# Optimization experiments

Hardware: AMD Instinct MI355X
Metric: run time of the kernel (lower is better)

The kernel has to match this reference:

```python
import jax, jax.numpy as jnp
import numpy as np

K = 9      # num_classes
A = 6      # anchors per location (A1 == A2 == 6)
C = 256    # fpn_out_channels


def conv3x3(x, w, b):
    # x: [N,C,H,W], w: [O,I,3,3], b: [O]
    y = jax.lax.conv_general_dilated(
        x, w, window_strides=(1, 1), padding='SAME',
        dimension_numbers=('NCHW', 'OIHW', 'NCHW'))
    return y + b[None, :, None, None]


def setup_inputs() -> dict:
    key = jax.random.key(0)
    ks = jax.random.split(key, 16)
    shapes = [(16, C, 64, 64), (16, C, 32, 32), (16, C, 16, 16),
              (16, C, 8, 8), (16, C, 4, 4), (16, C, 2, 2)]
    inp = {f'feat{i}': jax.random.normal(ks[i], s, dtype=jnp.float32)
           for i, s in enumerate(shapes)}
    # head 1 (used for pyramid levels 0,1) and head 2 (levels >=2)
    inp['w_reg1'] = jax.random.normal(ks[6], (4 * A, C, 3, 3), jnp.float32) * 0.05
    inp['b_reg1'] = jnp.zeros((4 * A,), jnp.float32)
    inp['w_cls1'] = jax.random.normal(ks[7], (K * A, C, 3, 3), jnp.float32) * 0.05
    inp['b_cls1'] = jnp.zeros((K * A,), jnp.float32)
    inp['w_reg2'] = jax.random.normal(ks[8], (4 * A, C, 3, 3), jnp.float32) * 0.05
    inp['b_reg2'] = jnp.zeros((4 * A,), jnp.float32)
    inp['w_cls2'] = jax.random.normal(ks[9], (K * A, C, 3, 3), jnp.float32) * 0.05
    inp['b_cls2'] = jnp.zeros((K * A,), jnp.float32)
    return inp


def reference(feat0, feat1, feat2, feat3, feat4, feat5,
              w_reg1, b_reg1, w_cls1, b_cls1,
              w_reg2, b_reg2, w_cls2, b_cls2):
    feats = [feat0, feat1, feat2, feat3, feat4, feat5]
    locations, confidences = [], []
    for i, x in enumerate(feats):
        if i < 2:
            wr, br, wc, bc = w_reg1, b_reg1, w_cls1, b_cls1
        else:
            wr, br, wc, bc = w_reg2, b_reg2, w_cls2, b_cls2
        n = x.shape[0]
        bbox_delta = conv3x3(x, wr, br).reshape(n, 4, -1)   # [N,4,A*H*W]
        bbox_conf = conv3x3(x, wc, bc).reshape(n, K, -1)    # [N,K,A*H*W]
        locations.append(bbox_delta)
        confidences.append(bbox_conf)
    bbox_delta = jnp.concatenate(locations, axis=2)
    confs = jnp.concatenate(confidences, axis=2)
    return bbox_delta, confs
```

## Files before the change

### kernel.cpp

```cpp
#include <hip/hip_runtime.h>
#include <hip/hip_bf16.h>


typedef float  f32x4  __attribute__((ext_vector_type(4)));
typedef short  bf16x8 __attribute__((ext_vector_type(8)));
typedef int    i32x4  __attribute__((ext_vector_type(4)));

#define TOTAL_ANCH 32760
#define BBOX_TOTAL 2096640
#define PW_BYTES   1474560
#define NB_MAIN    683

__device__ __forceinline__ unsigned short f2bf(float f) {
    unsigned u = __float_as_uint(f);
    return (unsigned short)((u + 0x7FFFu + ((u >> 16) & 1u)) >> 16);
}

__device__ __forceinline__ unsigned pack2(float a, float b) {
    return (unsigned)f2bf(a) | ((unsigned)f2bf(b) << 16);
}

__device__ __forceinline__ void gload16(const void* g, void* l) {
    __builtin_amdgcn_global_load_lds(
        (const __attribute__((address_space(1))) void*)g,
        (__attribute__((address_space(3))) void*)l, 16, 0, 0);
}

__global__ void retina_prepack(
    const float* __restrict__ wr1, const float* __restrict__ br1,
    const float* __restrict__ wc1, const float* __restrict__ bc1,
    const float* __restrict__ wr2, const float* __restrict__ br2,
    const float* __restrict__ wc2, const float* __restrict__ bc2,
    unsigned short* __restrict__ PW, float* __restrict__ PB)
{
    int g = blockIdx.x * 256 + threadIdx.x;
    if (g < 737280) {
        int e = g & 7;
        int b = (g >> 3) & 7;
        int q = g >> 6;
        int o = q % 80;
        int rest = q / 80;
        int kw = rest % 3; rest /= 3;
        int kh = rest % 3; rest /= 3;
        int chunk = rest & 3;
        int head  = rest >> 2;
        float v = 0.f;
        if (o < 78) {
            int c = (chunk << 6) + ((b ^ (o & 7)) << 3) + e;
            const float* wsrc; int oo;
            if (o < 24) { wsrc = head ? wr2 : wr1; oo = o; }
            else        { wsrc = head ? wc2 : wc1; oo = o - 24; }
            v = wsrc[((oo * 256 + c) * 3 + kh) * 3 + kw];
        }
        PW[g] = f2bf(v);
    }
    if (g < 160) {
        int head = g / 80, o = g % 80;
        float bv = 0.f;
        if (o < 24)      bv = (head ? br2 : br1)[o];
        else if (o < 78) bv = (head ? bc2 : bc1)[o - 24];
        PB[g] = bv;
    }
}

__global__ __launch_bounds__(256, 2) void retina_main(
    const float* __restrict__ f0, const float* __restrict__ f1,
    const float* __restrict__ f2, const float* __restrict__ f3,
    const float* __restrict__ f4, const float* __restrict__ f5,
    const unsigned short* __restrict__ PW, const float* __restrict__ PB,
    float* __restrict__ out)
{
    __shared__ __align__(16) char lds[32768 + 2 * 10240];

    const int tid = threadIdx.x;
    const int bid = blockIdx.x;

    int lvl, tile;
    if      (bid < 512) { lvl = 0; tile = bid;       }
    else if (bid < 640) { lvl = 1; tile = bid - 512; }
    else if (bid < 672) { lvl = 2; tile = bid - 640; }
    else if (bid < 680) { lvl = 3; tile = bid - 672; }
    else if (bid < 682) { lvl = 4; tile = bid - 680; }
    else                { lvl = 5; tile = 0;         }

    const int logW  = 6 - lvl;
    const int W     = 1 << logW;
    const int H     = W;
    const int logHW = 2 * logW;
    const int HW    = 1 << logHW;
    const int NHW   = 16 << logHW;

    const int nrowsTab[6] = {4, 6, 10, 18, 34, 34};
    const int offlTab[6]  = {0, 24576, 30720, 32256, 32640, 32736};
    const int S    = nrowsTab[lvl];
    const int offl = offlTab[lvl];
    const float* x = (lvl == 0) ? f0 : (lvl == 1) ? f1 : (lvl == 2) ? f2
                   : (lvl == 3) ? f3 : (lvl == 4) ? f4 : f5;
    const int head = (lvl < 2) ? 0 : 1;

    const int p0 = tile << 7;
    const int r0 = p0 >> logW;

    const int l   = tid & 63;
    const int wv  = tid >> 6;
    const int lg  = l >> 4;
    const int l16 = l & 15;

    int rlocal[2], wpos[2], hrow[2];
    #pragma unroll
    for (int nt = 0; nt < 2; ++nt) {
        int tpos   = wv * 32 + nt * 16 + l16;
        rlocal[nt] = tpos >> logW;
        wpos[nt]   = tpos & (W - 1);
        hrow[nt]   = (r0 + rlocal[nt]) & (H - 1);
    }

    f32x4 acc[5][2];
    {
        f32x4 zf = {0.f, 0.f, 0.f, 0.f};
        #pragma unroll
        for (int m = 0; m < 5; ++m) { acc[m][0] = zf; acc[m][1] = zf; }
    }

    const int axor  = l16 & 7;
    const int aoff0 = l16 * 128 + ((lg       ^ axor) << 4);
    const int aoff1 = l16 * 128 + (((4 + lg) ^ axor) << 4);

    const char* pwbase = (const char*)PW + (size_t)head * 368640;

    auto stageW = [&](int cidx, int buf) {
        const char* src = pwbase + (size_t)cidx * 10240 + wv * 2560 + l * 16;
        char*       dst = lds + 32768 + buf * 10240 + wv * 2560;
        gload16(src,        dst);
        gload16(src + 1024, dst + 1024);
        if (l < 32) gload16(src + 2048, dst + 2048);
    };

    auto stageX = [&](int chunk) {
        const int items = S << (logW + 3);
        for (int e = tid; e < items; e += 256) {
            int w = e & (W - 1);
            int b = (e >> logW) & 7;
            int s = e >> (logW + 3);
            int vr = r0 - 1 + s;
            i32x4 val = {0, 0, 0, 0};
            if ((unsigned)vr < (unsigned)(16 << logW)) {
                int n  = vr >> logW;
                int h  = vr & (H - 1);
                int c0 = (chunk << 6) + (b << 3);
                const float* src = x + (size_t)(((n << 8) + c0) << logHW) + (h << logW) + w;
                float v0 = src[0];          float v1 = src[(size_t)HW];
                float v2 = src[(size_t)2*HW]; float v3 = src[(size_t)3*HW];
                float v4 = src[(size_t)4*HW]; float v5 = src[(size_t)5*HW];
                float v6 = src[(size_t)6*HW]; float v7 = src[(size_t)7*HW];
                val[0] = (int)pack2(v0, v1);
                val[1] = (int)pack2(v2, v3);
                val[2] = (int)pack2(v4, v5);
                val[3] = (int)pack2(v6, v7);
            }
            int rowidx = (s << logW) + w;
            int boff   = rowidx * 128 + ((b ^ (rowidx & 7)) << 4);
            *(i32x4*)(lds + boff) = val;
        }
    };

    stageW(0, 0);
    stageX(0);
    __syncthreads();

    for (int chunk = 0; chunk < 4; ++chunk) {
        if (chunk) { stageX(chunk); __syncthreads(); }
        #pragma unroll
        for (int t9 = 0; t9 < 9; ++t9) {
            const int kh   = t9 / 3;
            const int kw   = t9 % 3;
            const int cidx = chunk * 9 + t9;

            if (cidx + 1 < 36) stageW(cidx + 1, (cidx + 1) & 1);

            bf16x8 bfr[2][2];
            #pragma unroll
            for (int nt = 0; nt < 2; ++nt) {
                int wp  = wpos[nt] + kw - 1;
                bool ok = ((unsigned)(hrow[nt] + kh - 1) < (unsigned)H)
                       && ((unsigned)wp < (unsigned)W);
                int wc = wp < 0 ? 0 : (wp >= W ? W - 1 : wp);
                int rowidx = ((rlocal[nt] + kh) << logW) + wc;
                int rsw = rowidx & 7;
                const char* bp = lds + rowidx * 128;
                bfr[nt][0] = *(const bf16x8*)(bp + ((lg       ^ rsw) << 4));
                bfr[nt][1] = *(const bf16x8*)(bp + (((4 + lg) ^ rsw) << 4));
                if (!ok) {
                    bf16x8 z = {0, 0, 0, 0, 0, 0, 0, 0};
                    bfr[nt][0] = z;
                    bfr[nt][1] = z;
                }
            }

            const char* wb = lds + 32768 + (cidx & 1) * 10240;
            #pragma unroll
            for (int m = 0; m < 5; ++m) {
                bf16x8 a0 = *(const bf16x8*)(wb + m * 2048 + aoff0);
                bf16x8 a1 = *(const bf16x8*)(wb + m * 2048 + aoff1);
                acc[m][0] = __builtin_amdgcn_mfma_f32_16x16x32_bf16(a0, bfr[0][0], acc[m][0], 0, 0, 0);
                acc[m][0] = __builtin_amdgcn_mfma_f32_16x16x32_bf16(a1, bfr[0][1], acc[m][0], 0, 0, 0);
                acc[m][1] = __builtin_amdgcn_mfma_f32_16x16x32_bf16(a0, bfr[1][0], acc[m][1], 0, 0, 0);
                acc[m][1] = __builtin_amdgcn_mfma_f32_16x16x32_bf16(a1, bfr[1][1], acc[m][1], 0, 0, 0);
            }
            __syncthreads();
        }
    }

    const float* bias = PB + head * 80;
    #pragma unroll
    for (int nt = 0; nt < 2; ++nt) {
        int pos = p0 + wv * 32 + nt * 16 + l16;
        if (pos >= NHW) continue;
        int n   = pos >> logHW;
        int rem = pos & (HW - 1);
        int base0 = offl + rem;
        #pragma unroll
        for (int m = 0; m < 5; ++m) {
            #pragma unroll
            for (int r = 0; r < 4; ++r) {
                int o = m * 16 + lg * 4 + r;
                if (o < 78) {
                    float v = acc[m][nt][r] + bias[o];
                    int idx;
                    if (o < 24) {
                        int g = o / 6, a = o - g * 6;
                        idx = (n * 4 + g) * TOTAL_ANCH + base0 + (a << logHW);
                    } else {
                        int cc = o - 24;
                        int k = cc / 6, a = cc - k * 6;
                        idx = BBOX_TOTAL + (n * 9 + k) * TOTAL_ANCH + base0 + (a << logHW);
                    }
                    out[idx] = v;
                }
            }
        }
    }
}

extern "C" void kernel_launch(void* const* d_in, const int* in_sizes, int n_in,
                              void* d_out, int out_size, void* d_ws, size_t ws_size,
                              hipStream_t stream) {
    const float* f0  = (const float*)d_in[0];
    const float* f1  = (const float*)d_in[1];
    const float* f2  = (const float*)d_in[2];
    const float* f3  = (const float*)d_in[3];
    const float* f4  = (const float*)d_in[4];
    const float* f5  = (const float*)d_in[5];
    const float* wr1 = (const float*)d_in[6];
    const float* br1 = (const float*)d_in[7];
    const float* wc1 = (const float*)d_in[8];
    const float* bc1 = (const float*)d_in[9];
    const float* wr2 = (const float*)d_in[10];
    const float* br2 = (const float*)d_in[11];
    const float* wc2 = (const float*)d_in[12];
    const float* bc2 = (const float*)d_in[13];

    unsigned short* PW = (unsigned short*)d_ws;
    float*          PB = (float*)((char*)d_ws + PW_BYTES);

    retina_prepack<<<2880, 256, 0, stream>>>(wr1, br1, wc1, bc1, wr2, br2, wc2, bc2, PW, PB);
    retina_main<<<NB_MAIN, 256, 0, stream>>>(f0, f1, f2, f3, f4, f5, PW, PB, (float*)d_out);
}
```

Measured before the change: 178.6 us.

## Stage weights two taps at a time with four LDS buffers, precompute B offsets

The weight pipeline now uses two sets of two LDS buffers, so each barrier interval handles two conv taps and prefetches the next two. This roughly halves the number of __syncthreads in the main loop. Per-tap LDS offsets and boundary masks for the input fragments are precomputed into registers before the loop instead of being recomputed each tap. The cost is 20KB more LDS per block, which may limit two blocks per CU, and extra registers for the 36 offset and mask values.

```diff
diff --git a/kernel.cpp b/kernel.cpp
--- a/kernel.cpp
+++ b/kernel.cpp
@@ -70,7 +70,7 @@
     const unsigned short* __restrict__ PW, const float* __restrict__ PB,
     float* __restrict__ out)
 {
-    __shared__ __align__(16) char lds[32768 + 2 * 10240];
+    __shared__ __align__(16) char lds[32768 + 4 * 10240];
 
     const int tid = threadIdx.x;
     const int bid = blockIdx.x;
@@ -113,6 +113,24 @@
         rlocal[nt] = tpos >> logW;
         wpos[nt]   = tpos & (W - 1);
         hrow[nt]   = (r0 + rlocal[nt]) & (H - 1);
+    }
+
+    int bofs0[2][9], bofs1[2][9];
+    bool bok[2][9];
+    #pragma unroll
+    for (int nt = 0; nt < 2; ++nt) {
+        #pragma unroll
+        for (int t9 = 0; t9 < 9; ++t9) {
+            int kh = t9 / 3, kw = t9 % 3;
+            int wp = wpos[nt] + kw - 1;
+            bok[nt][t9] = ((unsigned)(hrow[nt] + kh - 1) < (unsigned)H)
+                       && ((unsigned)wp < (unsigned)W);
+            int wc = wp < 0 ? 0 : (wp >= W ? W - 1 : wp);
+            int rowidx = ((rlocal[nt] + kh) << logW) + wc;
+            int rsw = rowidx & 7;
+            bofs0[nt][t9] = rowidx * 128 + ((lg       ^ rsw) << 4);
+            bofs1[nt][t9] = rowidx * 128 + (((4 + lg) ^ rsw) << 4);
+        }
     }
 
     f32x4 acc[5][2];
@@ -149,7 +167,7 @@
                 int h  = vr & (H - 1);
                 int c0 = (chunk << 6) + (b << 3);
                 const float* src = x + (size_t)(((n << 8) + c0) << logHW) + (h << logW) + w;
-                float v0 = src[0];          float v1 = src[(size_t)HW];
+                float v0 = src[0];            float v1 = src[(size_t)HW];
                 float v2 = src[(size_t)2*HW]; float v3 = src[(size_t)3*HW];
                 float v4 = src[(size_t)4*HW]; float v5 = src[(size_t)5*HW];
                 float v6 = src[(size_t)6*HW]; float v7 = src[(size_t)7*HW];
@@ -165,47 +183,50 @@
     };
 
     stageW(0, 0);
+    stageW(1, 1);
     stageX(0);
     __syncthreads();
 
     for (int chunk = 0; chunk < 4; ++chunk) {
         if (chunk) { stageX(chunk); __syncthreads(); }
-        #pragma unroll
-        for (int t9 = 0; t9 < 9; ++t9) {
-            const int kh   = t9 / 3;
-            const int kw   = t9 % 3;
-            const int cidx = chunk * 9 + t9;
-
-            if (cidx + 1 < 36) stageW(cidx + 1, (cidx + 1) & 1);
-
-            bf16x8 bfr[2][2];
+        const int set0 = (chunk * 5) & 1;
+        #pragma unroll
+        for (int iv = 0; iv < 5; ++iv) {
+            const int set  = set0 ^ (iv & 1);
+            const int c0   = chunk * 9 + iv * 2;
+            const int sz   = (iv == 4) ? 1 : 2;
+            const int pc   = chunk * 9 + ((iv == 4) ? 9 : iv * 2 + 2);
+            const int nPre = (iv == 3) ? 1 : 2;
+
+            if (pc < 36)              stageW(pc,     (set ^ 1) * 2 + 0);
+            if (nPre == 2 && pc + 1 < 36) stageW(pc + 1, (set ^ 1) * 2 + 1);
+
             #pragma unroll
-            for (int nt = 0; nt < 2; ++nt) {
-                int wp  = wpos[nt] + kw - 1;
-                bool ok = ((unsigned)(hrow[nt] + kh - 1) < (unsigned)H)
-                       && ((unsigned)wp < (unsigned)W);
-                int wc = wp < 0 ? 0 : (wp >= W ? W - 1 : wp);
-                int rowidx = ((rlocal[nt] + kh) << logW) + wc;
-                int rsw = rowidx & 7;
-                const char* bp = lds + rowidx * 128;
-                bfr[nt][0] = *(const bf16x8*)(bp + ((lg       ^ rsw) << 4));
-                bfr[nt][1] = *(const bf16x8*)(bp + (((4 + lg) ^ rsw) << 4));
-                if (!ok) {
-                    bf16x8 z = {0, 0, 0, 0, 0, 0, 0, 0};
-                    bfr[nt][0] = z;
-                    bfr[nt][1] = z;
+            for (int c2 = 0; c2 < 2; ++c2) {
+                if (c2 >= sz) break;
+                const int t9 = iv * 2 + c2;
+                bf16x8 bfr[2][2];
+                #pragma unroll
+                for (int nt = 0; nt < 2; ++nt) {
+                    const char* bp = lds;
+                    bfr[nt][0] = *(const bf16x8*)(bp + bofs0[nt][t9]);
+                    bfr[nt][1] = *(const bf16x8*)(bp + bofs1[nt][t9]);
+                    if (!bok[nt][t9]) {
+                        bf16x8 z = {0, 0, 0, 0, 0, 0, 0, 0};
+                        bfr[nt][0] = z;
+                        bfr[nt][1] = z;
+                    }
                 }
-            }
-
-            const char* wb = lds + 32768 + (cidx & 1) * 10240;
-            #pragma unroll
-            for (int m = 0; m < 5; ++m) {
-                bf16x8 a0 = *(const bf16x8*)(wb + m * 2048 + aoff0);
-                bf16x8 a1 = *(const bf16x8*)(wb + m * 2048 + aoff1);
-                acc[m][0] = __builtin_amdgcn_mfma_f32_16x16x32_bf16(a0, bfr[0][0], acc[m][0], 0, 0, 0);
-                acc[m][0] = __builtin_amdgcn_mfma_f32_16x16x32_bf16(a1, bfr[0][1], acc[m][0], 0, 0, 0);
-                acc[m][1] = __builtin_amdgcn_mfma_f32_16x16x32_bf16(a0, bfr[1][0], acc[m][1], 0, 0, 0);
-                acc[m][1] = __builtin_amdgcn_mfma_f32_16x16x32_bf16(a1, bfr[1][1], acc[m][1], 0, 0, 0);
+                const char* wb = lds + 32768 + (set * 2 + c2) * 10240;
+                #pragma unroll
+                for (int m = 0; m < 5; ++m) {
+                    bf16x8 a0 = *(const bf16x8*)(wb + m * 2048 + aoff0);
+                    bf16x8 a1 = *(const bf16x8*)(wb + m * 2048 + aoff1);
+                    acc[m][0] = __builtin_amdgcn_mfma_f32_16x16x32_bf16(a0, bfr[0][0], acc[m][0], 0, 0, 0);
+                    acc[m][0] = __builtin_amdgcn_mfma_f32_16x16x32_bf16(a1, bfr[0][1], acc[m][0], 0, 0, 0);
+                    acc[m][1] = __builtin_amdgcn_mfma_f32_16x16x32_bf16(a0, bfr[1][0], acc[m][1], 0, 0, 0);
+                    acc[m][1] = __builtin_amdgcn_mfma_f32_16x16x32_bf16(a1, bfr[1][1], acc[m][1], 0, 0, 0);
+                }
             }
             __syncthreads();
         }
```

Result: slower. 200.8 us (+12.4%).

## Load weight fragments directly into registers and drop LDS weight staging

Applied to the files above, without the earlier changes.

Weight fragments now go straight from global memory (L2-resident prepacked layout, swizzle removed) into registers, prefetched one tap ahead, instead of being double-buffered through LDS with global_load_lds. This removes the per-tap __syncthreads, so barriers only happen around the per-chunk input restaging. It also precomputes the B-operand LDS offsets and validity masks for all 9 taps once per thread. In exchange it adds register pressure (two sets of 10 A fragments plus 18 offsets) and redundant global/L2 reads of weights per wave, and it exposes global-load latency to each tap.

```diff
diff --git a/kernel.cpp b/kernel.cpp
--- a/kernel.cpp
+++ b/kernel.cpp
@@ -18,12 +18,6 @@
 
 __device__ __forceinline__ unsigned pack2(float a, float b) {
     return (unsigned)f2bf(a) | ((unsigned)f2bf(b) << 16);
-}
-
-__device__ __forceinline__ void gload16(const void* g, void* l) {
-    __builtin_amdgcn_global_load_lds(
-        (const __attribute__((address_space(1))) void*)g,
-        (__attribute__((address_space(3))) void*)l, 16, 0, 0);
 }
 
 __global__ void retina_prepack(
@@ -46,7 +40,7 @@
         int head  = rest >> 2;
         float v = 0.f;
         if (o < 78) {
-            int c = (chunk << 6) + ((b ^ (o & 7)) << 3) + e;
+            int c = (chunk << 6) + (b << 3) + e;
             const float* wsrc; int oo;
             if (o < 24) { wsrc = head ? wr2 : wr1; oo = o; }
             else        { wsrc = head ? wc2 : wc1; oo = o - 24; }
@@ -70,7 +64,7 @@
     const unsigned short* __restrict__ PW, const float* __restrict__ PB,
     float* __restrict__ out)
 {
-    __shared__ __align__(16) char lds[32768 + 2 * 10240];
+    __shared__ __align__(16) char lds[32768];
 
     const int tid = threadIdx.x;
     const int bid = blockIdx.x;
@@ -115,6 +109,24 @@
         hrow[nt]   = (r0 + rlocal[nt]) & (H - 1);
     }
 
+    int bofs0[2][9];
+    unsigned okb = 0;
+    #pragma unroll
+    for (int nt = 0; nt < 2; ++nt) {
+        #pragma unroll
+        for (int t9 = 0; t9 < 9; ++t9) {
+            int kh = t9 / 3, kw = t9 % 3;
+            int wp = wpos[nt] + kw - 1;
+            bool ok = ((unsigned)(hrow[nt] + kh - 1) < (unsigned)H)
+                   && ((unsigned)wp < (unsigned)W);
+            okb |= (unsigned)ok << (nt * 9 + t9);
+            int wc = wp < 0 ? 0 : (wp >= W ? W - 1 : wp);
+            int rowidx = ((rlocal[nt] + kh) << logW) + wc;
+            int rsw = rowidx & 7;
+            bofs0[nt][t9] = rowidx * 128 + ((lg ^ rsw) << 4);
+        }
+    }
+
     f32x4 acc[5][2];
     {
         f32x4 zf = {0.f, 0.f, 0.f, 0.f};
@@ -122,18 +134,16 @@
         for (int m = 0; m < 5; ++m) { acc[m][0] = zf; acc[m][1] = zf; }
     }
 
-    const int axor  = l16 & 7;
-    const int aoff0 = l16 * 128 + ((lg       ^ axor) << 4);
-    const int aoff1 = l16 * 128 + (((4 + lg) ^ axor) << 4);
-
     const char* pwbase = (const char*)PW + (size_t)head * 368640;
-
-    auto stageW = [&](int cidx, int buf) {
-        const char* src = pwbase + (size_t)cidx * 10240 + wv * 2560 + l * 16;
-        char*       dst = lds + 32768 + buf * 10240 + wv * 2560;
-        gload16(src,        dst);
-        gload16(src + 1024, dst + 1024);
-        if (l < 32) gload16(src + 2048, dst + 2048);
+    const char* abase  = pwbase + l16 * 128 + lg * 16;
+
+    auto loadA = [&](int cidx, bf16x8* A) {
+        const char* p = abase + (size_t)cidx * 10240;
+        #pragma unroll
+        for (int m = 0; m < 5; ++m) {
+            A[2 * m]     = *(const bf16x8*)(p + m * 2048);
+            A[2 * m + 1] = *(const bf16x8*)(p + m * 2048 + 64);
+        }
     };
 
     auto stageX = [&](int chunk) {
@@ -149,7 +159,7 @@
                 int h  = vr & (H - 1);
                 int c0 = (chunk << 6) + (b << 3);
                 const float* src = x + (size_t)(((n << 8) + c0) << logHW) + (h << logW) + w;
-                float v0 = src[0];          float v1 = src[(size_t)HW];
+                float v0 = src[0];            float v1 = src[(size_t)HW];
                 float v2 = src[(size_t)2*HW]; float v3 = src[(size_t)3*HW];
                 float v4 = src[(size_t)4*HW]; float v5 = src[(size_t)5*HW];
                 float v6 = src[(size_t)6*HW]; float v7 = src[(size_t)7*HW];
@@ -164,49 +174,47 @@
         }
     };
 
-    stageW(0, 0);
+    bf16x8 Ac[10];
+    loadA(0, Ac);
     stageX(0);
     __syncthreads();
 
     for (int chunk = 0; chunk < 4; ++chunk) {
-        if (chunk) { stageX(chunk); __syncthreads(); }
         #pragma unroll
         for (int t9 = 0; t9 < 9; ++t9) {
-            const int kh   = t9 / 3;
-            const int kw   = t9 % 3;
-            const int cidx = chunk * 9 + t9;
-
-            if (cidx + 1 < 36) stageW(cidx + 1, (cidx + 1) & 1);
+            const bool haveN = (t9 < 8) || (chunk < 3);
+            bf16x8 An[10];
+            if (haveN) loadA(chunk * 9 + t9 + 1, An);
 
             bf16x8 bfr[2][2];
             #pragma unroll
             for (int nt = 0; nt < 2; ++nt) {
-                int wp  = wpos[nt] + kw - 1;
-                bool ok = ((unsigned)(hrow[nt] + kh - 1) < (unsigned)H)
-                       && ((unsigned)wp < (unsigned)W);
-                int wc = wp < 0 ? 0 : (wp >= W ? W - 1 : wp);
-                int rowidx = ((rlocal[nt] + kh) << logW) + wc;
-                int rsw = rowidx & 7;
-                const char* bp = lds + rowidx * 128;
-                bfr[nt][0] = *(const bf16x8*)(bp + ((lg       ^ rsw) << 4));
-                bfr[nt][1] = *(const bf16x8*)(bp + (((4 + lg) ^ rsw) << 4));
-                if (!ok) {
+                int o0 = bofs0[nt][t9];
+                bfr[nt][0] = *(const bf16x8*)(lds + o0);
+                bfr[nt][1] = *(const bf16x8*)(lds + (o0 ^ 64));
+                if (!((okb >> (nt * 9 + t9)) & 1u)) {
                     bf16x8 z = {0, 0, 0, 0, 0, 0, 0, 0};
                     bfr[nt][0] = z;
                     bfr[nt][1] = z;
                 }
             }
 
-            const char* wb = lds + 32768 + (cidx & 1) * 10240;
             #pragma unroll
             for (int m = 0; m < 5; ++m) {
-                bf16x8 a0 = *(const bf16x8*)(wb + m * 2048 + aoff0);
-                bf16x8 a1 = *(const bf16x8*)(wb + m * 2048 + aoff1);
-                acc[m][0] = __builtin_amdgcn_mfma_f32_16x16x32_bf16(a0, bfr[0][0], acc[m][0], 0, 0, 0);
-                acc[m][0] = __builtin_amdgcn_mfma_f32_16x16x32_bf16(a1, bfr[0][1], acc[m][0], 0, 0, 0);
-                acc[m][1] = __builtin_amdgcn_mfma_f32_16x16x32_bf16(a0, bfr[1][0], acc[m][1], 0, 0, 0);
-                acc[m][1] = __builtin_amdgcn_mfma_f32_16x16x32_bf16(a1, bfr[1][1], acc[m][1], 0, 0, 0);
-            }
+                acc[m][0] = __builtin_amdgcn_mfma_f32_16x16x32_bf16(Ac[2*m],   bfr[0][0], acc[m][0], 0, 0, 0);
+                acc[m][0] = __builtin_amdgcn_mfma_f32_16x16x32_bf16(Ac[2*m+1], bfr[0][1], acc[m][0], 0, 0, 0);
+                acc[m][1] = __builtin_amdgcn_mfma_f32_16x16x32_bf16(Ac[2*m],   bfr[1][0], acc[m][1], 0, 0, 0);
+                acc[m][1] = __builtin_amdgcn_mfma_f32_16x16x32_bf16(Ac[2*m+1], bfr[1][1], acc[m][1], 0, 0, 0);
+            }
+
+            if (haveN) {
+                #pragma unroll
+                for (int i = 0; i < 10; ++i) Ac[i] = An[i];
+            }
+        }
+        if (chunk < 3) {
+            __syncthreads();
+            stageX(chunk + 1);
             __syncthreads();
         }
     }
@@ -223,7 +231,7 @@
         for (int m = 0; m < 5; ++m) {
             #pragma unroll
             for (int r = 0; r < 4; ++r) {
-                int o = m * 16 + lg * 4 + r;
+                int o = m * 16 + (l >> 4) * 4 + r;
                 if (o < 78) {
                     float v = acc[m][nt][r] + bias[o];
                     int idx;
```

After: 277.0 us. +55.1%, slower.

## Split K across wave pairs to reuse weight fragments over four N-tiles

Applied to the files above, without the earlier changes.

Each wave now covers 64 positions (four 16-column tiles) and only half of every 64-channel chunk, selected by wave index. Each weight fragment is loaded once and reused across four MFMAs, which cuts LDS reads of A per MFMA. Partial sums from the two wave pairs are combined through LDS after the main loop. Boundary masks are precomputed into a bitmask and rounding now uses the HIP bf16 intrinsic, at the cost of more accumulator registers and an extra reduction pass with a barrier.

```diff
diff --git a/kernel.cpp b/kernel.cpp
--- a/kernel.cpp
+++ b/kernel.cpp
@@ -12,8 +12,10 @@
 #define NB_MAIN    683
 
 __device__ __forceinline__ unsigned short f2bf(float f) {
-    unsigned u = __float_as_uint(f);
-    return (unsigned short)((u + 0x7FFFu + ((u >> 16) & 1u)) >> 16);
+    __hip_bfloat16 h = __float2bfloat16(f);
+    unsigned short u;
+    __builtin_memcpy(&u, &h, 2);
+    return u;
 }
 
 __device__ __forceinline__ unsigned pack2(float a, float b) {
@@ -105,26 +107,42 @@
     const int wv  = tid >> 6;
     const int lg  = l >> 4;
     const int l16 = l & 15;
-
-    int rlocal[2], wpos[2], hrow[2];
+    const int ph  = wv & 1;
+    const int kh2 = wv >> 1;
+    const int lgh = lg ^ (kh2 << 2);
+
+    int slotbase[4], wpos[4], hrow[4];
     #pragma unroll
-    for (int nt = 0; nt < 2; ++nt) {
-        int tpos   = wv * 32 + nt * 16 + l16;
-        rlocal[nt] = tpos >> logW;
-        wpos[nt]   = tpos & (W - 1);
-        hrow[nt]   = (r0 + rlocal[nt]) & (H - 1);
-    }
-
-    f32x4 acc[5][2];
+    for (int nt = 0; nt < 4; ++nt) {
+        int tpos     = ph * 64 + nt * 16 + l16;
+        int rl       = tpos >> logW;
+        slotbase[nt] = rl << logW;
+        wpos[nt]     = tpos & (W - 1);
+        hrow[nt]     = (r0 + rl) & (H - 1);
+    }
+
+    unsigned long long okb = 0;
+    #pragma unroll
+    for (int nt = 0; nt < 4; ++nt) {
+        #pragma unroll
+        for (int t9 = 0; t9 < 9; ++t9) {
+            int kh = t9 / 3, kw = t9 % 3;
+            bool ok = ((unsigned)(hrow[nt] + kh - 1) < (unsigned)H)
+                   && ((unsigned)(wpos[nt] + kw - 1) < (unsigned)W);
+            okb |= (unsigned long long)ok << (nt * 9 + t9);
+        }
+    }
+
+    f32x4 acc[5][4];
     {
         f32x4 zf = {0.f, 0.f, 0.f, 0.f};
         #pragma unroll
-        for (int m = 0; m < 5; ++m) { acc[m][0] = zf; acc[m][1] = zf; }
-    }
-
-    const int axor  = l16 & 7;
-    const int aoff0 = l16 * 128 + ((lg       ^ axor) << 4);
-    const int aoff1 = l16 * 128 + (((4 + lg) ^ axor) << 4);
+        for (int m = 0; m < 5; ++m)
+            #pragma unroll
+            for (int nt = 0; nt < 4; ++nt) acc[m][nt] = zf;
+    }
+
+    const int aoffB = l16 * 128 + ((lgh ^ (l16 & 7)) << 4);
 
     const char* pwbase = (const char*)PW + (size_t)head * 368640;
 
@@ -149,7 +167,7 @@
                 int h  = vr & (H - 1);
                 int c0 = (chunk << 6) + (b << 3);
                 const float* src = x + (size_t)(((n << 8) + c0) << logHW) + (h << logW) + w;
-                float v0 = src[0];          float v1 = src[(size_t)HW];
+                float v0 = src[0];            float v1 = src[(size_t)HW];
                 float v2 = src[(size_t)2*HW]; float v3 = src[(size_t)3*HW];
                 float v4 = src[(size_t)4*HW]; float v5 = src[(size_t)5*HW];
                 float v6 = src[(size_t)6*HW]; float v7 = src[(size_t)7*HW];
@@ -169,73 +187,84 @@
     __syncthreads();
 
     for (int chunk = 0; chunk < 4; ++chunk) {
-        if (chunk) { stageX(chunk); __syncthreads(); }
         #pragma unroll
         for (int t9 = 0; t9 < 9; ++t9) {
-            const int kh   = t9 / 3;
-            const int kw   = t9 % 3;
             const int cidx = chunk * 9 + t9;
+            const int kh = t9 / 3, kw = t9 % 3;
 
             if (cidx + 1 < 36) stageW(cidx + 1, (cidx + 1) & 1);
 
-            bf16x8 bfr[2][2];
-            #pragma unroll
-            for (int nt = 0; nt < 2; ++nt) {
-                int wp  = wpos[nt] + kw - 1;
-                bool ok = ((unsigned)(hrow[nt] + kh - 1) < (unsigned)H)
-                       && ((unsigned)wp < (unsigned)W);
-                int wc = wp < 0 ? 0 : (wp >= W ? W - 1 : wp);
-                int rowidx = ((rlocal[nt] + kh) << logW) + wc;
-                int rsw = rowidx & 7;
-                const char* bp = lds + rowidx * 128;
-                bfr[nt][0] = *(const bf16x8*)(bp + ((lg       ^ rsw) << 4));
-                bfr[nt][1] = *(const bf16x8*)(bp + (((4 + lg) ^ rsw) << 4));
-                if (!ok) {
+            const char* wb = lds + 32768 + (cidx & 1) * 10240;
+            bf16x8 Afr[5];
+            #pragma unroll
+            for (int m = 0; m < 5; ++m)
+                Afr[m] = *(const bf16x8*)(wb + m * 2048 + aoffB);
+
+            #pragma unroll
+            for (int nt = 0; nt < 4; ++nt) {
+                int rowidx = slotbase[nt] + (kh << logW) + ((wpos[nt] + kw - 1) & (W - 1));
+                int boff   = rowidx * 128 + ((lgh ^ (rowidx & 7)) << 4);
+                bf16x8 b = *(const bf16x8*)(lds + boff);
+                if (!((okb >> (nt * 9 + t9)) & 1ull)) {
                     bf16x8 z = {0, 0, 0, 0, 0, 0, 0, 0};
-                    bfr[nt][0] = z;
-                    bfr[nt][1] = z;
+                    b = z;
                 }
-            }
-
-            const char* wb = lds + 32768 + (cidx & 1) * 10240;
-            #pragma unroll
-            for (int m = 0; m < 5; ++m) {
-                bf16x8 a0 = *(const bf16x8*)(wb + m * 2048 + aoff0);
-                bf16x8 a1 = *(const bf16x8*)(wb + m * 2048 + aoff1);
-                acc[m][0] = __builtin_amdgcn_mfma_f32_16x16x32_bf16(a0, bfr[0][0], acc[m][0], 0, 0, 0);
-                acc[m][0] = __builtin_amdgcn_mfma_f32_16x16x32_bf16(a1, bfr[0][1], acc[m][0], 0, 0, 0);
-                acc[m][1] = __builtin_amdgcn_mfma_f32_16x16x32_bf16(a0, bfr[1][0], acc[m][1], 0, 0, 0);
-                acc[m][1] = __builtin_amdgcn_mfma_f32_16x16x32_bf16(a1, bfr[1][1], acc[m][1], 0, 0, 0);
+                #pragma unroll
+                for (int m = 0; m < 5; ++m)
+                    acc[m][nt] = __builtin_amdgcn_mfma_f32_16x16x32_bf16(Afr[m], b, acc[m][nt], 0, 0, 0);
             }
             __syncthreads();
         }
-    }
-
-    const float* bias = PB + head * 80;
-    #pragma unroll
-    for (int nt = 0; nt < 2; ++nt) {
-        int pos = p0 + wv * 32 + nt * 16 + l16;
-        if (pos >= NHW) continue;
-        int n   = pos >> logHW;
-        int rem = pos & (HW - 1);
-        int base0 = offl + rem;
-        #pragma unroll
-        for (int m = 0; m < 5; ++m) {
-            #pragma unroll
-            for (int r = 0; r < 4; ++r) {
-                int o = m * 16 + lg * 4 + r;
-                if (o < 78) {
-                    float v = acc[m][nt][r] + bias[o];
-                    int idx;
-                    if (o < 24) {
-                        int g = o / 6, a = o - g * 6;
-                        idx = (n * 4 + g) * TOTAL_ANCH + base0 + (a << logHW);
-                    } else {
-                        int cc = o - 24;
-                        int k = cc / 6, a = cc - k * 6;
-                        idx = BBOX_TOTAL + (n * 9 + k) * TOTAL_ANCH + base0 + (a << logHW);
+        if (chunk < 3) {
+            stageX(chunk + 1);
+            __syncthreads();
+        }
+    }
+
+    if (wv >= 2) {
+        char* red = lds + (wv - 2) * 20480;
+        #pragma unroll
+        for (int m = 0; m < 5; ++m)
+            #pragma unroll
+            for (int nt = 0; nt < 4; ++nt)
+                *(f32x4*)(red + (m * 4 + nt) * 1024 + l * 16) = acc[m][nt];
+    }
+    __syncthreads();
+
+    if (wv < 2) {
+        const char* red = lds + wv * 20480;
+        #pragma unroll
+        for (int m = 0; m < 5; ++m)
+            #pragma unroll
+            for (int nt = 0; nt < 4; ++nt)
+                acc[m][nt] += *(const f32x4*)(red + (m * 4 + nt) * 1024 + l * 16);
+
+        const float* bias = PB + head * 80;
+        #pragma unroll
+        for (int nt = 0; nt < 4; ++nt) {
+            int pos = p0 + wv * 64 + nt * 16 + l16;
+            if (pos >= NHW) continue;
+            int n   = pos >> logHW;
+            int rem = pos & (HW - 1);
+            int base0 = offl + rem;
+            #pragma unroll
+            for (int m = 0; m < 5; ++m) {
+                #pragma unroll
+                for (int r = 0; r < 4; ++r) {
+                    int o = m * 16 + lg * 4 + r;
+                    if (o < 78) {
+                        float v = acc[m][nt][r] + bias[o];
+                        int idx;
+                        if (o < 24) {
+                            int g = o / 6, a = o - g * 6;
+                            idx = (n * 4 + g) * TOTAL_ANCH + base0 + (a << logHW);
+                        } else {
+                            int cc = o - 24;
+                            int k = cc / 6, a = cc - k * 6;
+                            idx = BBOX_TOTAL + (n * 9 + k) * TOTAL_ANCH + base0 + (a << logHW);
+                        }
+                        out[idx] = v;
                     }
-                    out[idx] = v;
                 }
             }
         }
```

Result: slower. 208.9 us (+17.0%).
